# Kernel optimization log

Measured on AMD Instinct MI355X. Metric: run time of the kernel, lower is better.

The kernel has to match this reference:

```python
import jax, jax.numpy as jnp
import numpy as np

PATCH = 16
EMB = 16
HID = 1024
B, S = 128, 4096
PAD_IDX = S  # max_sequence_length
PMAX = S // PATCH  # 256 patches max per sample
IN_DIM = PATCH + PATCH * EMB  # 272


def setup_inputs() -> dict:
    key = jax.random.key(0)
    ks = jax.random.split(key, 8)
    lengths = jax.random.randint(ks[0], (B,), 1, S + 1).astype(jnp.int32)
    vals = jax.random.normal(ks[1], (B, S), dtype=jnp.float32)
    # prefix-of-ones validity mask in the last feature channel
    mask = (jnp.arange(S)[None, :] < lengths[:, None]).astype(jnp.float32)
    x = jnp.stack([vals, mask], axis=-1)  # [B, S, 2]
    sc1 = 1.0 / np.sqrt(IN_DIM)
    sc2 = 1.0 / np.sqrt(HID)
    return {
        "x": x,
        "lengths": lengths,
        "pos_table": jax.random.normal(ks[2], (S + 1, EMB), dtype=jnp.float32),
        "W1": jax.random.uniform(ks[3], (IN_DIM, HID), jnp.float32, -sc1, sc1),
        "b1": jax.random.uniform(ks[4], (HID,), jnp.float32, -sc1, sc1),
        "W2": jax.random.uniform(ks[5], (HID, HID), jnp.float32, -sc2, sc2),
        "b2": jax.random.uniform(ks[6], (HID,), jnp.float32, -sc2, sc2),
    }


def reference(x, lengths, pos_table, W1, b1, W2, b2):
    # x: [B, S, 2] (value, mask); lengths[i] == mask[i].sum()
    t = jnp.arange(S)  # padded timeline, T = PMAX * PATCH == S
    vl = lengths[:, None]  # [B, 1]
    # pad each series to a multiple of PATCH by repeating its last valid value
    gather_idx = jnp.minimum(t[None, :], jnp.maximum(vl - 1, 0))  # [B, S]
    vals = jnp.take_along_axis(x[:, :, 0], gather_idx, axis=1)  # [B, S]
    pos = jnp.where(t[None, :] < vl, t[None, :], PAD_IDX)  # [B, S]
    vals_p = vals.reshape(B, PMAX, PATCH)
    pos_emb = pos_table[pos].reshape(B, PMAX, PATCH * EMB)  # gather + flatten
    feat = jnp.concatenate([vals_p, pos_emb], axis=-1)  # [B, PMAX, 272]
    h = jax.nn.gelu(feat @ W1 + b1, approximate=False)
    out = h @ W2 + b2  # [B, PMAX, HID]
    n_patch = (lengths + PATCH - 1) // PATCH  # [B]
    patch_mask = jnp.arange(PMAX)[None, :] < n_patch[:, None]
    out = out * patch_mask[:, :, None]  # zero rows beyond patch_cnt
    return out, n_patch
```

## Files before the change

kernel.cpp:

```cpp
#include <hip/hip_runtime.h>
#include <hip/hip_bf16.h>
#include <math.h>

#define NB     128
#define SLEN   4096
#define HID_   1024
#define INDIM_ 272
#define KPAD_  320
#define MFULL  32768
#define N_     1024

typedef __bf16 bf16x8 __attribute__((ext_vector_type(8)));
typedef float  f32x4  __attribute__((ext_vector_type(4)));
typedef __hip_bfloat16 hb;


__global__ void prep_w(const float* __restrict__ W1, const float* __restrict__ W2,
                       hb* __restrict__ w1t, hb* __restrict__ w2t) {
    __shared__ float tt[64][65];
    const int kt = blockIdx.x;
    const int nt = blockIdx.y;
    const int c = threadIdx.x & 63, r4 = threadIdx.x >> 6;
    if (kt < 5) {
#pragma unroll
        for (int j = 0; j < 16; ++j) {
            int r = j * 4 + r4;
            int k = kt * 64 + r;
            tt[r][c] = (k < INDIM_) ? W1[k * 1024 + nt * 64 + c] : 0.0f;
        }
        __syncthreads();
#pragma unroll
        for (int j = 0; j < 16; ++j) {
            int r = j * 4 + r4;
            w1t[(nt * 64 + r) * KPAD_ + kt * 64 + c] = __float2bfloat16(tt[c][r]);
        }
    } else {
        const int kw = kt - 5;
#pragma unroll
        for (int j = 0; j < 16; ++j) {
            int r = j * 4 + r4;
            tt[r][c] = W2[(kw * 64 + r) * 1024 + nt * 64 + c];
        }
        __syncthreads();
#pragma unroll
        for (int j = 0; j < 16; ++j) {
            int r = j * 4 + r4;
            w2t[(nt * 64 + r) * 1024 + kw * 64 + c] = __float2bfloat16(tt[c][r]);
        }
    }
}

__global__ __launch_bounds__(512) void build_feat_c(const float* __restrict__ x,
                                                    const int* __restrict__ lengths,
                                                    const float* __restrict__ pos_table,
                                                    hb* __restrict__ feat,
                                                    unsigned short* __restrict__ rowmap,
                                                    int* __restrict__ mc,
                                                    float* __restrict__ np_out,
                                                    float* __restrict__ out) {
    __shared__ int scan[NB];
    const int b = blockIdx.x, t = threadIdx.x;
    if (t < NB) scan[t] = (lengths[t] + 15) >> 4;
    __syncthreads();
    for (int d = 1; d < NB; d <<= 1) {
        int v = 0;
        if (t < NB && t >= d) v = scan[t - d];
        __syncthreads();
        if (t < NB && t >= d) scan[t] += v;
        __syncthreads();
    }
    const int L = lengths[b];
    const int np = (L + 15) >> 4;
    const int off = scan[b] - np;
    if (b == 0) {
        if (t < NB) np_out[t] = (float)((lengths[t] + 15) >> 4);
        if (t == 0) *mc = scan[NB - 1];
    }
    for (int p = t; p < np; p += 512)
        rowmap[off + p] = (unsigned short)(b * 256 + p);

    const float* xb = x + (long)b * SLEN * 2;
    const int total = np * 40;
    for (int c = t; c < total; c += 512) {
        const int p = c / 40;
        const int j = c - p * 40;
        const int col = j * 8;
        bf16x8 v;
        if (j < 2) {
#pragma unroll
            for (int e = 0; e < 8; ++e) {
                int tt2 = p * 16 + j * 8 + e;
                int idx = (tt2 < L) ? tt2 : (L - 1);
                v[e] = (__bf16)xb[(long)idx * 2];
            }
        } else if (col < INDIM_) {
            const int q = col - 16;
            const int tt2 = p * 16 + (q >> 4);
            const int pt = (tt2 < L) ? tt2 : SLEN;
            const float* src = pos_table + pt * 16 + (q & 15);
#pragma unroll
            for (int e = 0; e < 8; ++e) v[e] = (__bf16)src[e];
        } else {
            v = (bf16x8)0;
        }
        *(bf16x8*)(feat + (long)(off + p) * KPAD_ + col) = v;
    }

    float* ob = out + (long)b * 256 * N_;
    const int nzero = (256 - np) * 256;
    for (int i = t; i < nzero; i += 512) {
        const int p = np + (i >> 8);
        const int c4 = i & 255;
        *(f32x4*)(ob + (long)p * N_ + c4 * 4) = (f32x4)0.0f;
    }
}


__device__ __forceinline__ void gl_lds16(const hb* g, hb* l) {
    __builtin_amdgcn_global_load_lds(
        (const __attribute__((address_space(1))) unsigned int*)g,
        (__attribute__((address_space(3))) unsigned int*)l, 16, 0, 0);
}

__device__ __forceinline__ float gelu_tanh(float v) {
    float u = 1.5957691216f * v * (1.0f + 0.044715f * v * v);
    float e = __expf(u);
    float th = (e - 1.0f) / (e + 1.0f);
    return 0.5f * v * (1.0f + th);
}

template <int MODE>
__global__ __launch_bounds__(512, 2) void gemm256(const hb* __restrict__ A,
                                                  const hb* __restrict__ BT,
                                                  const float* __restrict__ bias,
                                                  const unsigned short* __restrict__ rowmap,
                                                  const int* __restrict__ mc,
                                                  hb* __restrict__ HOut,
                                                  float* __restrict__ FOut,
                                                  int K, int nt) {
    __shared__ __align__(16) hb Sh[4][16384];

    const int Mc = *mc;
    const int activeBm = (Mc + 255) >> 8;
    const int nActive = activeBm * 4;
    const int bid = blockIdx.x;
    if (bid >= nActive) return;
    const int q = nActive >> 3, r = nActive & 7;
    const int xcd = bid & 7, idx = bid >> 3;
    const int wg = (xcd < r ? xcd * (q + 1) : r * (q + 1) + (xcd - r) * q) + idx;
    const int bm = wg >> 2;
    const int bn = wg & 3;

    const int tid = threadIdx.x;
    const int wid = tid >> 6, lane = tid & 63;
    const int wr = wid >> 2, wc = wid & 3;
    const int fr = lane & 15, kg = lane >> 4;
    const int swz = (fr & 7) << 4;

    const long arow0 = (long)bm * 256;
    const int  brow0 = bn * 256;
    const hb* Bbase = BT + (long)brow0 * K;

    const int srow = tid >> 3;
    const int sel  = (((tid & 7) << 4) ^ ((srow & 7) << 4)) >> 1;
    const int ldst = tid * 8;

    f32x4 acc[8][4] = {};

    auto stage = [&](int t, int bsel) {
        const int k0 = t << 6;
#pragma unroll
        for (int j = 0; j < 4; ++j) {
            long gr = arow0 + j * 64 + srow;
            if (gr >= Mc) gr = Mc - 1;
            gl_lds16(A + gr * K + k0 + sel, &Sh[bsel][j * 4096 + ldst]);
        }
#pragma unroll
        for (int j = 0; j < 4; ++j)
            gl_lds16(Bbase + (long)(j * 64 + srow) * K + k0 + sel,
                     &Sh[2 + bsel][j * 4096 + ldst]);
    };

    stage(0, 0);
    stage(1, 1);
    asm volatile("s_waitcnt vmcnt(8)" ::: "memory");
    asm volatile("s_barrier" ::: "memory");

#define LDA_(dst, Ab, half)                                                  \
    _Pragma("unroll") for (int i = 0; i < 4; ++i)                            \
    _Pragma("unroll") for (int ks = 0; ks < 2; ++ks)                         \
        dst[i][ks] = *(const bf16x8*)((Ab) +                                 \
            (wr * 128 + (half) * 64 + i * 16 + fr) * 128 +                   \
            ((ks * 64 + kg * 16) ^ swz));

#define LDB_(Bb, half)                                                       \
    _Pragma("unroll") for (int jn = 0; jn < 2; ++jn)                         \
    _Pragma("unroll") for (int ks = 0; ks < 2; ++ks)                         \
        Bf[half][jn][ks] = *(const bf16x8*)((Bb) +                           \
            (wc * 64 + (half) * 32 + jn * 16 + fr) * 128 +                   \
            ((ks * 64 + kg * 16) ^ swz));

#define MFMA_QUAD(Aarr, a, b)                                                \
    __builtin_amdgcn_s_setprio(1);                                           \
    _Pragma("unroll") for (int ks = 0; ks < 2; ++ks)                         \
    _Pragma("unroll") for (int i = 0; i < 4; ++i)                            \
    _Pragma("unroll") for (int jn = 0; jn < 2; ++jn)                         \
        acc[(a) * 4 + i][(b) * 2 + jn] =                                     \
            __builtin_amdgcn_mfma_f32_16x16x32_bf16(                         \
                Aarr[i][ks], Bf[b][jn][ks], acc[(a) * 4 + i][(b) * 2 + jn],  \
                0, 0, 0);                                                    \
    __builtin_amdgcn_s_setprio(0);

    for (int t = 0; t < nt; ++t) {
        const char* Ab = (const char*)(&Sh[t & 1][0]);
        const char* Bb = (const char*)(&Sh[2 + (t & 1)][0]);
        bf16x8 A0[4][2], A1[4][2], Bf[2][2][2];

        LDB_(Bb, 0)
        LDA_(A0, Ab, 0)
        MFMA_QUAD(A0, 0, 0)
        LDB_(Bb, 1)
        MFMA_QUAD(A0, 0, 1)
        LDA_(A1, Ab, 1)
        MFMA_QUAD(A1, 1, 1)
        asm volatile("s_waitcnt lgkmcnt(0)" ::: "memory");
        asm volatile("s_barrier" ::: "memory");
        if (t + 2 < nt) stage(t + 2, t & 1);
        MFMA_QUAD(A1, 1, 0)
        if (t + 1 < nt) {
            if (t + 2 < nt) {
                asm volatile("s_waitcnt vmcnt(8)" ::: "memory");
            } else {
                asm volatile("s_waitcnt vmcnt(0)" ::: "memory");
            }
            asm volatile("s_barrier" ::: "memory");
        }
    }

    const int rbase = wr * 128 + kg * 4;
    const int cbase = wc * 64 + fr;
    float bvv[4];
#pragma unroll
    for (int ni = 0; ni < 4; ++ni) bvv[ni] = bias[bn * 256 + cbase + ni * 16];

    if (MODE == 0) {
        hb* Cs = (hb*)Sh;
#pragma unroll
        for (int ni = 0; ni < 4; ++ni) {
            const int col = cbase + ni * 16;
#pragma unroll
            for (int mi = 0; mi < 8; ++mi)
#pragma unroll
                for (int r2 = 0; r2 < 4; ++r2) {
                    float v = acc[mi][ni][r2] + bvv[ni];
                    Cs[(rbase + mi * 16 + r2) * 256 + col] = __float2bfloat16(gelu_tanh(v));
                }
        }
        __syncthreads();
        const hb* Cl = (const hb*)Sh;
#pragma unroll
        for (int c = 0; c < 16; ++c) {
            const int e = (c * 512 + tid) * 8;
            const int row = e >> 8, col = e & 255;
            bf16x8 v = *(const bf16x8*)(Cl + e);
            *(bf16x8*)(HOut + (arow0 + row) * N_ + bn * 256 + col) = v;
        }
    } else {
        float* Cf = (float*)Sh;
#pragma unroll
        for (int half = 0; half < 2; ++half) {
            if (half) __syncthreads();
            if ((wc >> 1) == half) {
#pragma unroll
                for (int ni = 0; ni < 4; ++ni) {
                    const int col = cbase + ni * 16 - half * 128;
#pragma unroll
                    for (int mi = 0; mi < 8; ++mi)
#pragma unroll
                        for (int r2 = 0; r2 < 4; ++r2)
                            Cf[(rbase + mi * 16 + r2) * 128 + col] =
                                acc[mi][ni][r2] + bvv[ni];
                }
            }
            __syncthreads();
#pragma unroll
            for (int c = 0; c < 16; ++c) {
                const int e = (c * 512 + tid) * 4;
                const int row = e >> 7, col = e & 127;
                const long cidx = arow0 + row;
                if (cidx < Mc) {
                    f32x4 v = *(const f32x4*)(Cf + e);
                    *(f32x4*)(FOut + (long)rowmap[cidx] * N_ + bn * 256 + half * 128 + col) = v;
                }
            }
        }
    }
}


extern "C" void kernel_launch(void* const* d_in, const int* in_sizes, int n_in,
                              void* d_out, int out_size, void* d_ws, size_t ws_size,
                              hipStream_t stream) {
    const float* x         = (const float*)d_in[0];
    const int*   lengths   = (const int*)d_in[1];
    const float* pos_table = (const float*)d_in[2];
    const float* W1        = (const float*)d_in[3];
    const float* b1        = (const float*)d_in[4];
    const float* W2        = (const float*)d_in[5];
    const float* b2        = (const float*)d_in[6];
    float* out = (float*)d_out;

    char* ws = (char*)d_ws;
    hb* w1t                = (hb*)(ws);
    hb* w2t                = (hb*)(ws + 655360);
    hb* feat               = (hb*)(ws + 2752512);
    hb* h                  = (hb*)(ws + 23724032);
    unsigned short* rowmap = (unsigned short*)(ws + 90832896);
    int* mc                = (int*)(ws + 90898432);

    hipLaunchKernelGGL(prep_w, dim3(21, 16), dim3(256), 0, stream, W1, W2, w1t, w2t);
    hipLaunchKernelGGL(build_feat_c, dim3(NB), dim3(512), 0, stream,
                       x, lengths, pos_table, feat, rowmap, mc,
                       out + (long)MFULL * N_, out);

    hipLaunchKernelGGL((gemm256<0>), dim3(512), dim3(512), 0, stream,
                       feat, w1t, b1, rowmap, mc, h, nullptr, KPAD_, KPAD_ / 64);
    hipLaunchKernelGGL((gemm256<1>), dim3(512), dim3(512), 0, stream,
                       h, w2t, b2, rowmap, mc, nullptr, out, HID_, HID_ / 64);
}
```

Baseline: 100.8 us.

## Shrink GEMM tiles to 128x128 and split output zero-fill into its own kernel

Both GEMM kernels move from 256x256 tiles with 512 threads to 128x128 tiles with 256 threads. Each wave now holds half as many accumulators, the grid grows fourfold, and the FP32 epilogue no longer needs two halves. The zeroing of padded output rows moves out of build_feat_c into a separate row-parallel kernel so the feature build does less serial work. The cost is less operand reuse per tile, more global and LDS traffic per FLOP, and one extra kernel launch.

```diff
diff --git a/kernel.cpp b/kernel.cpp
--- a/kernel.cpp
+++ b/kernel.cpp
@@ -56,8 +56,7 @@
                                                     hb* __restrict__ feat,
                                                     unsigned short* __restrict__ rowmap,
                                                     int* __restrict__ mc,
-                                                    float* __restrict__ np_out,
-                                                    float* __restrict__ out) {
+                                                    float* __restrict__ np_out) {
     __shared__ int scan[NB];
     const int b = blockIdx.x, t = threadIdx.x;
     if (t < NB) scan[t] = (lengths[t] + 15) >> 4;
@@ -105,13 +104,15 @@
         }
         *(bf16x8*)(feat + (long)(off + p) * KPAD_ + col) = v;
     }
-
-    float* ob = out + (long)b * 256 * N_;
-    const int nzero = (256 - np) * 256;
-    for (int i = t; i < nzero; i += 512) {
-        const int p = np + (i >> 8);
-        const int c4 = i & 255;
-        *(f32x4*)(ob + (long)p * N_ + c4 * 4) = (f32x4)0.0f;
+}
+
+__global__ __launch_bounds__(256) void zero_fill(const int* __restrict__ lengths,
+                                                 float* __restrict__ out) {
+    for (int r = blockIdx.x; r < MFULL; r += 512) {
+        const int b = r >> 8, p = r & 255;
+        const int np = (lengths[b] + 15) >> 4;
+        if (p >= np)
+            *(f32x4*)(out + (long)r * N_ + threadIdx.x * 4) = (f32x4)0.0f;
     }
 }
 
@@ -130,7 +131,7 @@
 }
 
 template <int MODE>
-__global__ __launch_bounds__(512, 2) void gemm256(const hb* __restrict__ A,
+__global__ __launch_bounds__(256, 2) void gemm128(const hb* __restrict__ A,
                                                   const hb* __restrict__ BT,
                                                   const float* __restrict__ bias,
                                                   const unsigned short* __restrict__ rowmap,
@@ -138,47 +139,46 @@
                                                   hb* __restrict__ HOut,
                                                   float* __restrict__ FOut,
                                                   int K, int nt) {
-    __shared__ __align__(16) hb Sh[4][16384];
+    __shared__ __align__(16) hb Sh[4][8192];
 
     const int Mc = *mc;
-    const int activeBm = (Mc + 255) >> 8;
-    const int nActive = activeBm * 4;
+    const int nActive = ((Mc + 127) >> 7) * 8;
     const int bid = blockIdx.x;
     if (bid >= nActive) return;
     const int q = nActive >> 3, r = nActive & 7;
     const int xcd = bid & 7, idx = bid >> 3;
     const int wg = (xcd < r ? xcd * (q + 1) : r * (q + 1) + (xcd - r) * q) + idx;
-    const int bm = wg >> 2;
-    const int bn = wg & 3;
+    const int bm = wg >> 3;
+    const int bn = wg & 7;
 
     const int tid = threadIdx.x;
     const int wid = tid >> 6, lane = tid & 63;
-    const int wr = wid >> 2, wc = wid & 3;
+    const int wr = wid >> 1, wc = wid & 1;
     const int fr = lane & 15, kg = lane >> 4;
     const int swz = (fr & 7) << 4;
 
-    const long arow0 = (long)bm * 256;
-    const int  brow0 = bn * 256;
+    const long arow0 = (long)bm * 128;
+    const int  brow0 = bn * 128;
     const hb* Bbase = BT + (long)brow0 * K;
 
     const int srow = tid >> 3;
     const int sel  = (((tid & 7) << 4) ^ ((srow & 7) << 4)) >> 1;
     const int ldst = tid * 8;
 
-    f32x4 acc[8][4] = {};
+    f32x4 acc[4][4] = {};
 
     auto stage = [&](int t, int bsel) {
         const int k0 = t << 6;
 #pragma unroll
         for (int j = 0; j < 4; ++j) {
-            long gr = arow0 + j * 64 + srow;
+            long gr = arow0 + j * 32 + srow;
             if (gr >= Mc) gr = Mc - 1;
-            gl_lds16(A + gr * K + k0 + sel, &Sh[bsel][j * 4096 + ldst]);
+            gl_lds16(A + gr * K + k0 + sel, &Sh[bsel][j * 2048 + ldst]);
         }
 #pragma unroll
         for (int j = 0; j < 4; ++j)
-            gl_lds16(Bbase + (long)(j * 64 + srow) * K + k0 + sel,
-                     &Sh[2 + bsel][j * 4096 + ldst]);
+            gl_lds16(Bbase + (long)(j * 32 + srow) * K + k0 + sel,
+                     &Sh[2 + bsel][j * 2048 + ldst]);
     };
 
     stage(0, 0);
@@ -187,10 +187,10 @@
     asm volatile("s_barrier" ::: "memory");
 
 #define LDA_(dst, Ab, half)                                                  \
-    _Pragma("unroll") for (int i = 0; i < 4; ++i)                            \
+    _Pragma("unroll") for (int i = 0; i < 2; ++i)                            \
     _Pragma("unroll") for (int ks = 0; ks < 2; ++ks)                         \
         dst[i][ks] = *(const bf16x8*)((Ab) +                                 \
-            (wr * 128 + (half) * 64 + i * 16 + fr) * 128 +                   \
+            (wr * 64 + (half) * 32 + i * 16 + fr) * 128 +                    \
             ((ks * 64 + kg * 16) ^ swz));
 
 #define LDB_(Bb, half)                                                       \
@@ -203,18 +203,18 @@
 #define MFMA_QUAD(Aarr, a, b)                                                \
     __builtin_amdgcn_s_setprio(1);                                           \
     _Pragma("unroll") for (int ks = 0; ks < 2; ++ks)                         \
-    _Pragma("unroll") for (int i = 0; i < 4; ++i)                            \
+    _Pragma("unroll") for (int i = 0; i < 2; ++i)                            \
     _Pragma("unroll") for (int jn = 0; jn < 2; ++jn)                         \
-        acc[(a) * 4 + i][(b) * 2 + jn] =                                     \
+        acc[(a) * 2 + i][(b) * 2 + jn] =                                     \
             __builtin_amdgcn_mfma_f32_16x16x32_bf16(                         \
-                Aarr[i][ks], Bf[b][jn][ks], acc[(a) * 4 + i][(b) * 2 + jn],  \
+                Aarr[i][ks], Bf[b][jn][ks], acc[(a) * 2 + i][(b) * 2 + jn],  \
                 0, 0, 0);                                                    \
     __builtin_amdgcn_s_setprio(0);
 
     for (int t = 0; t < nt; ++t) {
         const char* Ab = (const char*)(&Sh[t & 1][0]);
         const char* Bb = (const char*)(&Sh[2 + (t & 1)][0]);
-        bf16x8 A0[4][2], A1[4][2], Bf[2][2][2];
+        bf16x8 A0[2][2], A1[2][2], Bf[2][2][2];
 
         LDB_(Bb, 0)
         LDA_(A0, Ab, 0)
@@ -237,11 +237,11 @@
         }
     }
 
-    const int rbase = wr * 128 + kg * 4;
+    const int rbase = wr * 64 + kg * 4;
     const int cbase = wc * 64 + fr;
     float bvv[4];
 #pragma unroll
-    for (int ni = 0; ni < 4; ++ni) bvv[ni] = bias[bn * 256 + cbase + ni * 16];
+    for (int ni = 0; ni < 4; ++ni) bvv[ni] = bias[bn * 128 + cbase + ni * 16];
 
     if (MODE == 0) {
         hb* Cs = (hb*)Sh;
@@ -249,49 +249,41 @@
         for (int ni = 0; ni < 4; ++ni) {
             const int col = cbase + ni * 16;
 #pragma unroll
-            for (int mi = 0; mi < 8; ++mi)
+            for (int mi = 0; mi < 4; ++mi)
 #pragma unroll
                 for (int r2 = 0; r2 < 4; ++r2) {
                     float v = acc[mi][ni][r2] + bvv[ni];
-                    Cs[(rbase + mi * 16 + r2) * 256 + col] = __float2bfloat16(gelu_tanh(v));
+                    Cs[(rbase + mi * 16 + r2) * 128 + col] = __float2bfloat16(gelu_tanh(v));
                 }
         }
         __syncthreads();
-        const hb* Cl = (const hb*)Sh;
-#pragma unroll
-        for (int c = 0; c < 16; ++c) {
-            const int e = (c * 512 + tid) * 8;
-            const int row = e >> 8, col = e & 255;
-            bf16x8 v = *(const bf16x8*)(Cl + e);
-            *(bf16x8*)(HOut + (arow0 + row) * N_ + bn * 256 + col) = v;
+#pragma unroll
+        for (int c = 0; c < 8; ++c) {
+            const int e = (c * 256 + tid) * 8;
+            const int row = e >> 7, col = e & 127;
+            bf16x8 v = *(const bf16x8*)(Cs + e);
+            *(bf16x8*)(HOut + (arow0 + row) * N_ + bn * 128 + col) = v;
         }
     } else {
         float* Cf = (float*)Sh;
 #pragma unroll
-        for (int half = 0; half < 2; ++half) {
-            if (half) __syncthreads();
-            if ((wc >> 1) == half) {
-#pragma unroll
-                for (int ni = 0; ni < 4; ++ni) {
-                    const int col = cbase + ni * 16 - half * 128;
-#pragma unroll
-                    for (int mi = 0; mi < 8; ++mi)
-#pragma unroll
-                        for (int r2 = 0; r2 < 4; ++r2)
-                            Cf[(rbase + mi * 16 + r2) * 128 + col] =
-                                acc[mi][ni][r2] + bvv[ni];
-                }
-            }
-            __syncthreads();
-#pragma unroll
-            for (int c = 0; c < 16; ++c) {
-                const int e = (c * 512 + tid) * 4;
-                const int row = e >> 7, col = e & 127;
-                const long cidx = arow0 + row;
-                if (cidx < Mc) {
-                    f32x4 v = *(const f32x4*)(Cf + e);
-                    *(f32x4*)(FOut + (long)rowmap[cidx] * N_ + bn * 256 + half * 128 + col) = v;
-                }
+        for (int ni = 0; ni < 4; ++ni) {
+            const int col = cbase + ni * 16;
+#pragma unroll
+            for (int mi = 0; mi < 4; ++mi)
+#pragma unroll
+                for (int r2 = 0; r2 < 4; ++r2)
+                    Cf[(rbase + mi * 16 + r2) * 128 + col] = acc[mi][ni][r2] + bvv[ni];
+        }
+        __syncthreads();
+#pragma unroll
+        for (int c = 0; c < 16; ++c) {
+            const int e = (c * 256 + tid) * 4;
+            const int row = e >> 7, col = e & 127;
+            const long cidx = arow0 + row;
+            if (cidx < Mc) {
+                f32x4 v = *(const f32x4*)(Cf + e);
+                *(f32x4*)(FOut + (long)rowmap[cidx] * N_ + bn * 128 + col) = v;
             }
         }
     }
@@ -320,11 +312,11 @@
 
     hipLaunchKernelGGL(prep_w, dim3(21, 16), dim3(256), 0, stream, W1, W2, w1t, w2t);
     hipLaunchKernelGGL(build_feat_c, dim3(NB), dim3(512), 0, stream,
-                       x, lengths, pos_table, feat, rowmap, mc,
-                       out + (long)MFULL * N_, out);
-
-    hipLaunchKernelGGL((gemm256<0>), dim3(512), dim3(512), 0, stream,
+                       x, lengths, pos_table, feat, rowmap, mc, out + (long)MFULL * N_);
+    hipLaunchKernelGGL(zero_fill, dim3(512), dim3(256), 0, stream, lengths, out);
+
+    hipLaunchKernelGGL((gemm128<0>), dim3(2048), dim3(256), 0, stream,
                        feat, w1t, b1, rowmap, mc, h, nullptr, KPAD_, KPAD_ / 64);
-    hipLaunchKernelGGL((gemm256<1>), dim3(512), dim3(512), 0, stream,
+    hipLaunchKernelGGL((gemm128<1>), dim3(2048), dim3(256), 0, stream,
                        h, w2t, b2, rowmap, mc, nullptr, out, HID_, HID_ / 64);
 }
```

After: 111.2 us. +10.3%, slower.

## Interleave GEMM loads in eight phases and move output zeroing into second GEMM

Applied to the files above, without the earlier changes.

Restructures the GEMM main loop so that A and B tile loads are split into half-tiles and interleaved between the four MFMA quadrants, with barriers between phases (an 8-phase schedule). A is now prefetched one step ahead and B two steps ahead. The zero-fill of padded output rows moves from the feature-build kernel into 512 extra blocks of the second GEMM launch, so it can run alongside the GEMM blocks. This adds many more barriers per iteration, and the extra zeroing blocks compete with GEMM blocks for the same compute units.

```diff
diff --git a/kernel.cpp b/kernel.cpp
--- a/kernel.cpp
+++ b/kernel.cpp
@@ -56,8 +56,7 @@
                                                     hb* __restrict__ feat,
                                                     unsigned short* __restrict__ rowmap,
                                                     int* __restrict__ mc,
-                                                    float* __restrict__ np_out,
-                                                    float* __restrict__ out) {
+                                                    float* __restrict__ np_out) {
     __shared__ int scan[NB];
     const int b = blockIdx.x, t = threadIdx.x;
     if (t < NB) scan[t] = (lengths[t] + 15) >> 4;
@@ -105,14 +104,6 @@
         }
         *(bf16x8*)(feat + (long)(off + p) * KPAD_ + col) = v;
     }
-
-    float* ob = out + (long)b * 256 * N_;
-    const int nzero = (256 - np) * 256;
-    for (int i = t; i < nzero; i += 512) {
-        const int p = np + (i >> 8);
-        const int c4 = i & 255;
-        *(f32x4*)(ob + (long)p * N_ + c4 * 4) = (f32x4)0.0f;
-    }
 }
 
 
@@ -129,21 +120,42 @@
     return 0.5f * v * (1.0f + th);
 }
 
+#define BARRIER() asm volatile("s_barrier" ::: "memory")
+#define LGKM0()   asm volatile("s_waitcnt lgkmcnt(0)" ::: "memory")
+#define LGKM8()   asm volatile("s_waitcnt lgkmcnt(8)" ::: "memory")
+#define VMCNT(n)  asm volatile("s_waitcnt vmcnt(" #n ")" ::: "memory")
+
 template <int MODE>
-__global__ __launch_bounds__(512, 2) void gemm256(const hb* __restrict__ A,
-                                                  const hb* __restrict__ BT,
-                                                  const float* __restrict__ bias,
-                                                  const unsigned short* __restrict__ rowmap,
-                                                  const int* __restrict__ mc,
-                                                  hb* __restrict__ HOut,
-                                                  float* __restrict__ FOut,
-                                                  int K, int nt) {
+__global__ __launch_bounds__(512, 2) void gemm8p(const hb* __restrict__ A,
+                                                 const hb* __restrict__ BT,
+                                                 const float* __restrict__ bias,
+                                                 const unsigned short* __restrict__ rowmap,
+                                                 const int* __restrict__ mc,
+                                                 const int* __restrict__ lengths,
+                                                 hb* __restrict__ HOut,
+                                                 float* __restrict__ FOut,
+                                                 int K, int nt) {
     __shared__ __align__(16) hb Sh[4][16384];
+
+    const int tid = threadIdx.x;
+    const int bid = blockIdx.x;
+
+    if (MODE == 1 && bid >= 512) {
+        const int zb = bid - 512;
+        const int half = tid >> 8;
+        const int c4 = tid & 255;
+        for (int r = zb * 2 + half; r < MFULL; r += 1024) {
+            const int b = r >> 8, p = r & 255;
+            const int np = (lengths[b] + 15) >> 4;
+            if (p >= np)
+                *(f32x4*)(FOut + (long)r * N_ + c4 * 4) = (f32x4)0.0f;
+        }
+        return;
+    }
 
     const int Mc = *mc;
     const int activeBm = (Mc + 255) >> 8;
     const int nActive = activeBm * 4;
-    const int bid = blockIdx.x;
     if (bid >= nActive) return;
     const int q = nActive >> 3, r = nActive & 7;
     const int xcd = bid & 7, idx = bid >> 3;
@@ -151,7 +163,6 @@
     const int bm = wg >> 2;
     const int bn = wg & 3;
 
-    const int tid = threadIdx.x;
     const int wid = tid >> 6, lane = tid & 63;
     const int wr = wid >> 2, wc = wid & 3;
     const int fr = lane & 15, kg = lane >> 4;
@@ -163,77 +174,90 @@
 
     const int srow = tid >> 3;
     const int sel  = (((tid & 7) << 4) ^ ((srow & 7) << 4)) >> 1;
-    const int ldst = tid * 8;
+    const int lofs = (tid & 7) * 8;
 
     f32x4 acc[8][4] = {};
 
-    auto stage = [&](int t, int bsel) {
-        const int k0 = t << 6;
-#pragma unroll
-        for (int j = 0; j < 4; ++j) {
-            long gr = arow0 + j * 64 + srow;
+    auto stageA = [&](int t, int h) {
+        const int buf = t & 1, k0 = t << 6;
+#pragma unroll
+        for (int j = 0; j < 2; ++j) {
+            const int row = h * 128 + j * 64 + srow;
+            long gr = arow0 + row;
             if (gr >= Mc) gr = Mc - 1;
-            gl_lds16(A + gr * K + k0 + sel, &Sh[bsel][j * 4096 + ldst]);
-        }
-#pragma unroll
-        for (int j = 0; j < 4; ++j)
-            gl_lds16(Bbase + (long)(j * 64 + srow) * K + k0 + sel,
-                     &Sh[2 + bsel][j * 4096 + ldst]);
+            gl_lds16(A + gr * K + k0 + sel, &Sh[buf][row * 64 + lofs]);
+        }
     };
-
-    stage(0, 0);
-    stage(1, 1);
-    asm volatile("s_waitcnt vmcnt(8)" ::: "memory");
-    asm volatile("s_barrier" ::: "memory");
-
-#define LDA_(dst, Ab, half)                                                  \
-    _Pragma("unroll") for (int i = 0; i < 4; ++i)                            \
+    auto stageB = [&](int t, int h) {
+        const int buf = 2 + (t & 1), k0 = t << 6;
+#pragma unroll
+        for (int j = 0; j < 2; ++j) {
+            const int row = h * 128 + j * 64 + srow;
+            gl_lds16(Bbase + (long)row * K + k0 + sel, &Sh[buf][row * 64 + lofs]);
+        }
+    };
+
+    stageA(0, 0); stageA(0, 1);
+    stageB(0, 0); stageB(0, 1);
+    if (nt > 1) { stageB(1, 0); stageB(1, 1); }
+    VMCNT(4);
+    BARRIER();
+
+#define LDA_Q(qa)                                                            \
+    _Pragma("unroll") for (int mi = 0; mi < 4; ++mi)                         \
     _Pragma("unroll") for (int ks = 0; ks < 2; ++ks)                         \
-        dst[i][ks] = *(const bf16x8*)((Ab) +                                 \
-            (wr * 128 + (half) * 64 + i * 16 + fr) * 128 +                   \
+        Af[mi][ks] = *(const bf16x8*)(Ab +                                   \
+            (wr * 128 + (qa) * 64 + mi * 16 + fr) * 128 +                    \
             ((ks * 64 + kg * 16) ^ swz));
 
-#define LDB_(Bb, half)                                                       \
+#define LDB_Q(qb)                                                            \
     _Pragma("unroll") for (int jn = 0; jn < 2; ++jn)                         \
     _Pragma("unroll") for (int ks = 0; ks < 2; ++ks)                         \
-        Bf[half][jn][ks] = *(const bf16x8*)((Bb) +                           \
-            (wc * 64 + (half) * 32 + jn * 16 + fr) * 128 +                   \
+        Bf[qb][jn][ks] = *(const bf16x8*)(Bb +                               \
+            (wc * 64 + (qb) * 32 + jn * 16 + fr) * 128 +                     \
             ((ks * 64 + kg * 16) ^ swz));
 
-#define MFMA_QUAD(Aarr, a, b)                                                \
+#define MFMA16(qa, qb)                                                       \
     __builtin_amdgcn_s_setprio(1);                                           \
     _Pragma("unroll") for (int ks = 0; ks < 2; ++ks)                         \
-    _Pragma("unroll") for (int i = 0; i < 4; ++i)                            \
+    _Pragma("unroll") for (int mi = 0; mi < 4; ++mi)                         \
     _Pragma("unroll") for (int jn = 0; jn < 2; ++jn)                         \
-        acc[(a) * 4 + i][(b) * 2 + jn] =                                     \
+        acc[(qa) * 4 + mi][(qb) * 2 + jn] =                                  \
             __builtin_amdgcn_mfma_f32_16x16x32_bf16(                         \
-                Aarr[i][ks], Bf[b][jn][ks], acc[(a) * 4 + i][(b) * 2 + jn],  \
+                Af[mi][ks], Bf[qb][jn][ks], acc[(qa) * 4 + mi][(qb) * 2 + jn],\
                 0, 0, 0);                                                    \
     __builtin_amdgcn_s_setprio(0);
 
     for (int t = 0; t < nt; ++t) {
         const char* Ab = (const char*)(&Sh[t & 1][0]);
         const char* Bb = (const char*)(&Sh[2 + (t & 1)][0]);
-        bf16x8 A0[4][2], A1[4][2], Bf[2][2][2];
-
-        LDB_(Bb, 0)
-        LDA_(A0, Ab, 0)
-        MFMA_QUAD(A0, 0, 0)
-        LDB_(Bb, 1)
-        MFMA_QUAD(A0, 0, 1)
-        LDA_(A1, Ab, 1)
-        MFMA_QUAD(A1, 1, 1)
-        asm volatile("s_waitcnt lgkmcnt(0)" ::: "memory");
-        asm volatile("s_barrier" ::: "memory");
-        if (t + 2 < nt) stage(t + 2, t & 1);
-        MFMA_QUAD(A1, 1, 0)
+        bf16x8 Af[4][2], Bf[2][2][2];
+        const bool sA = (t + 1 < nt);
+        const bool sB = (t + 2 < nt);
+
+        LDB_Q(0)
+        LDA_Q(0)
+        if (sA) stageA(t + 1, 0);
+        LGKM8();
+        BARRIER(); LGKM0();
+        MFMA16(0, 0)
+        BARRIER();
+        LDB_Q(1)
+        if (sA) stageA(t + 1, 1);
+        BARRIER(); LGKM0();
+        MFMA16(0, 1)
+        BARRIER();
+        LDA_Q(1)
+        if (sB) stageB(t + 2, 0);
+        BARRIER(); LGKM0();
+        MFMA16(1, 1)
+        BARRIER();
+        if (sB) stageB(t + 2, 1);
+        BARRIER();
+        MFMA16(1, 0)
         if (t + 1 < nt) {
-            if (t + 2 < nt) {
-                asm volatile("s_waitcnt vmcnt(8)" ::: "memory");
-            } else {
-                asm volatile("s_waitcnt vmcnt(0)" ::: "memory");
-            }
-            asm volatile("s_barrier" ::: "memory");
+            if (t + 2 < nt) { VMCNT(4); } else { VMCNT(0); }
+            BARRIER();
         }
     }
 
@@ -245,6 +269,7 @@
 
     if (MODE == 0) {
         hb* Cs = (hb*)Sh;
+        __syncthreads();
 #pragma unroll
         for (int ni = 0; ni < 4; ++ni) {
             const int col = cbase + ni * 16;
@@ -269,7 +294,7 @@
         float* Cf = (float*)Sh;
 #pragma unroll
         for (int half = 0; half < 2; ++half) {
-            if (half) __syncthreads();
+            __syncthreads();
             if ((wc >> 1) == half) {
 #pragma unroll
                 for (int ni = 0; ni < 4; ++ni) {
@@ -320,11 +345,10 @@
 
     hipLaunchKernelGGL(prep_w, dim3(21, 16), dim3(256), 0, stream, W1, W2, w1t, w2t);
     hipLaunchKernelGGL(build_feat_c, dim3(NB), dim3(512), 0, stream,
-                       x, lengths, pos_table, feat, rowmap, mc,
-                       out + (long)MFULL * N_, out);
-
-    hipLaunchKernelGGL((gemm256<0>), dim3(512), dim3(512), 0, stream,
-                       feat, w1t, b1, rowmap, mc, h, nullptr, KPAD_, KPAD_ / 64);
-    hipLaunchKernelGGL((gemm256<1>), dim3(512), dim3(512), 0, stream,
-                       h, w2t, b2, rowmap, mc, nullptr, out, HID_, HID_ / 64);
-}
+                       x, lengths, pos_table, feat, rowmap, mc, out + (long)MFULL * N_);
+
+    hipLaunchKernelGGL((gemm8p<0>), dim3(512), dim3(512), 0, stream,
+                       feat, w1t, b1, rowmap, mc, lengths, h, nullptr, KPAD_, KPAD_ / 64);
+    hipLaunchKernelGGL((gemm8p<1>), dim3(1024), dim3(512), 0, stream,
+                       h, w2t, b2, rowmap, mc, lengths, nullptr, out, HID_, HID_ / 64);
+}
```

Result: slower. 113.0 us (+12.1%).

## Split feature build across patch chunks and move output zeroing into GEMM2 extra blocks

Applied to the files above, without the earlier changes.

The feature-building kernel now launches four blocks per sample, each handling a 64-patch chunk, instead of one block per sample, so it has more parallelism. Zeroing of padded output rows moves from that kernel into 512 extra blocks appended to the second GEMM launch. Those extra blocks write zeros while the GEMM blocks compute, overlapping the zero-fill with matrix work. The cost is the redundant prefix scan in every chunk block, and the zeroing blocks may compete with GEMM blocks for CUs and memory bandwidth.

```diff
diff --git a/kernel.cpp b/kernel.cpp
--- a/kernel.cpp
+++ b/kernel.cpp
@@ -56,10 +56,10 @@
                                                     hb* __restrict__ feat,
                                                     unsigned short* __restrict__ rowmap,
                                                     int* __restrict__ mc,
-                                                    float* __restrict__ np_out,
-                                                    float* __restrict__ out) {
+                                                    float* __restrict__ np_out) {
     __shared__ int scan[NB];
     const int b = blockIdx.x, t = threadIdx.x;
+    const int chunk = blockIdx.y;
     if (t < NB) scan[t] = (lengths[t] + 15) >> 4;
     __syncthreads();
     for (int d = 1; d < NB; d <<= 1) {
@@ -72,18 +72,23 @@
     const int L = lengths[b];
     const int np = (L + 15) >> 4;
     const int off = scan[b] - np;
-    if (b == 0) {
+    if (b == 0 && chunk == 0) {
         if (t < NB) np_out[t] = (float)((lengths[t] + 15) >> 4);
         if (t == 0) *mc = scan[NB - 1];
     }
-    for (int p = t; p < np; p += 512)
+    const int p0 = chunk * 64;
+    const int p1 = min(np, p0 + 64);
+    if (p0 >= p1) return;
+    const int cnt = p1 - p0;
+
+    for (int p = p0 + t; p < p1; p += 512)
         rowmap[off + p] = (unsigned short)(b * 256 + p);
 
     const float* xb = x + (long)b * SLEN * 2;
-    const int total = np * 40;
+    const int total = cnt * 40;
     for (int c = t; c < total; c += 512) {
-        const int p = c / 40;
-        const int j = c - p * 40;
+        const int p = p0 + c / 40;
+        const int j = c - (c / 40) * 40;
         const int col = j * 8;
         bf16x8 v;
         if (j < 2) {
@@ -105,14 +110,6 @@
         }
         *(bf16x8*)(feat + (long)(off + p) * KPAD_ + col) = v;
     }
-
-    float* ob = out + (long)b * 256 * N_;
-    const int nzero = (256 - np) * 256;
-    for (int i = t; i < nzero; i += 512) {
-        const int p = np + (i >> 8);
-        const int c4 = i & 255;
-        *(f32x4*)(ob + (long)p * N_ + c4 * 4) = (f32x4)0.0f;
-    }
 }
 
 
@@ -135,15 +132,31 @@
                                                   const float* __restrict__ bias,
                                                   const unsigned short* __restrict__ rowmap,
                                                   const int* __restrict__ mc,
+                                                  const int* __restrict__ lengths,
                                                   hb* __restrict__ HOut,
                                                   float* __restrict__ FOut,
                                                   int K, int nt) {
     __shared__ __align__(16) hb Sh[4][16384];
 
+    const int tid = threadIdx.x;
+    const int bid = blockIdx.x;
+
+    if (MODE == 1 && bid >= 512) {
+        const int zb = bid - 512;
+        const int half = tid >> 8;
+        const int c4 = tid & 255;
+        for (int r = zb * 2 + half; r < MFULL; r += 1024) {
+            const int b = r >> 8, p = r & 255;
+            const int np = (lengths[b] + 15) >> 4;
+            if (p >= np)
+                *(f32x4*)(FOut + (long)r * N_ + c4 * 4) = (f32x4)0.0f;
+        }
+        return;
+    }
+
     const int Mc = *mc;
     const int activeBm = (Mc + 255) >> 8;
     const int nActive = activeBm * 4;
-    const int bid = blockIdx.x;
     if (bid >= nActive) return;
     const int q = nActive >> 3, r = nActive & 7;
     const int xcd = bid & 7, idx = bid >> 3;
@@ -151,7 +164,6 @@
     const int bm = wg >> 2;
     const int bn = wg & 3;
 
-    const int tid = threadIdx.x;
     const int wid = tid >> 6, lane = tid & 63;
     const int wr = wid >> 2, wc = wid & 3;
     const int fr = lane & 15, kg = lane >> 4;
@@ -319,12 +331,11 @@
     int* mc                = (int*)(ws + 90898432);
 
     hipLaunchKernelGGL(prep_w, dim3(21, 16), dim3(256), 0, stream, W1, W2, w1t, w2t);
-    hipLaunchKernelGGL(build_feat_c, dim3(NB), dim3(512), 0, stream,
-                       x, lengths, pos_table, feat, rowmap, mc,
-                       out + (long)MFULL * N_, out);
+    hipLaunchKernelGGL(build_feat_c, dim3(NB, 4), dim3(512), 0, stream,
+                       x, lengths, pos_table, feat, rowmap, mc, out + (long)MFULL * N_);
 
     hipLaunchKernelGGL((gemm256<0>), dim3(512), dim3(512), 0, stream,
-                       feat, w1t, b1, rowmap, mc, h, nullptr, KPAD_, KPAD_ / 64);
-    hipLaunchKernelGGL((gemm256<1>), dim3(512), dim3(512), 0, stream,
-                       h, w2t, b2, rowmap, mc, nullptr, out, HID_, HID_ / 64);
-}
+                       feat, w1t, b1, rowmap, mc, lengths, h, nullptr, KPAD_, KPAD_ / 64);
+    hipLaunchKernelGGL((gemm256<1>), dim3(1024), dim3(512), 0, stream,
+                       h, w2t, b2, rowmap, mc, lengths, nullptr, out, HID_, HID_ / 64);
+}
```

After: 102.6 us. Within noise of the previous version (+1.8%).
